# Performance work log

Hardware: AMD Instinct MI355X
Metric: run time of the kernel (lower is better)

Reference implementation:

```python
import jax, jax.numpy as jnp
import numpy as np

EPS = 1e-12  # torch F.normalize eps

def _l2norm(v, axis):
    n = jnp.linalg.norm(v, axis=axis, keepdims=True)
    return v / jnp.maximum(n, EPS)

def setup_inputs() -> dict:
    key = jax.random.key(0)
    k1, k2, k3 = jax.random.split(key, 3)
    N, D, H, W, K = 32, 512, 40, 40, 64
    x = jax.random.normal(k1, (N, D, H, W), dtype=jnp.float32)
    conv_weight = jax.random.normal(k2, (K, D), dtype=jnp.float32) * 0.05
    centroids = jax.random.uniform(k3, (K, D), dtype=jnp.float32)
    return {"x": x, "conv_weight": conv_weight, "centroids": centroids}

def reference(x, conv_weight, centroids):
    N, D, H, W = x.shape
    K = centroids.shape[0]
    # descriptor-wise L2 normalization over channel dim
    x = _l2norm(x, axis=1)
    x_flat = x.reshape(N, D, H * W)                       # [N, D, S]
    # 1x1 conv == per-pixel linear: [K,D] @ [N,D,S] -> [N,K,S]
    logits = jnp.einsum('kd,nds->nks', conv_weight, x_flat)
    soft_assign = jax.nn.softmax(logits, axis=1)          # softmax over clusters
    # vlad[n,k,d] = sum_s a[n,k,s] * (x[n,d,s] - c[k,d])
    #            = (a @ x^T) - (sum_s a) * c   -- two GEMM-like ops, no K-loop
    agg = jnp.einsum('nks,nds->nkd', soft_assign, x_flat)  # [N, K, D]
    a_sum = soft_assign.sum(axis=2)                        # [N, K]
    vlad = agg - a_sum[:, :, None] * centroids[None, :, :]
    # intra-normalization over D, flatten, global L2 normalization
    vlad = _l2norm(vlad, axis=2)
    vlad = vlad.reshape(N, K * D)
    vlad = _l2norm(vlad, axis=1)
    return vlad
```

## Files before the change

kernel.cpp:

```cpp
#include <hip/hip_runtime.h>
#include <math.h>

#define N_ 32
#define D_ 512
#define S_ 1600
#define K_ 64

typedef __attribute__((ext_vector_type(8))) short short8;
typedef __attribute__((ext_vector_type(4))) short short4v;
typedef __attribute__((ext_vector_type(4))) float f32x4;
typedef __attribute__((ext_vector_type(2))) unsigned u32x2;

static __device__ __forceinline__ short f2bf(float f) {
    unsigned u = __float_as_uint(f);
    u += 0x7fffu + ((u >> 16) & 1u);
    return (short)(u >> 16);
}
static __device__ __forceinline__ unsigned pk2(float a, float b) {
    return (unsigned)(unsigned short)f2bf(a) | ((unsigned)(unsigned short)f2bf(b) << 16);
}

__global__ __launch_bounds__(256) void kW(const float* __restrict__ w,
                                          short* __restrict__ w16)
{
    int i4 = (blockIdx.x * 256 + threadIdx.x) * 4;
    float4 v = *(const float4*)&w[i4];
    short4 h = {f2bf(v.x), f2bf(v.y), f2bf(v.z), f2bf(v.w)};
    *(short4*)&w16[i4] = h;
}

__global__ __launch_bounds__(256) void kA(const float* __restrict__ x,
                                          const short* __restrict__ w16,
                                          short* __restrict__ aprime,
                                          float* __restrict__ asum)
{
    __shared__ short T[2][64 * 64];
    __shared__ float invSS[64];
    __shared__ float wredS[4][66];

    const int tid = threadIdx.x;
    const int wv  = tid >> 6;
    const int l   = tid & 63;
    const int lk  = l & 15;
    const int q   = l >> 4;
    const int n   = blockIdx.x / 25;
    const int s0  = (blockIdx.x % 25) * 64;

    const float* xb = x + (size_t)n * D_ * S_;
    const float* xrow = xb + (size_t)(4 * wv + q) * S_ + s0 + 4 * lk;
    const int row   = 4 * lk + q;
    const int rswz  = row & 15;

    float ssql[4] = {0.f, 0.f, 0.f, 0.f};
    f32x4 accl[4];
#pragma unroll
    for (int st = 0; st < 4; ++st) accl[st] = (f32x4){0.f, 0.f, 0.f, 0.f};

    if (tid < 64) invSS[tid] = 0.f;

#define STAGE(c, b)                                                          \
    {                                                                        \
        float4 v[4];                                                         \
        _Pragma("unroll")                                                    \
        for (int jj = 0; jj < 4; ++jj)                                       \
            v[jj] = *(const float4*)&xrow[(size_t)(64 * (c) + 16 * jj) * S_];\
        _Pragma("unroll")                                                    \
        for (int jj = 0; jj < 4; ++jj) {                                     \
            ssql[0] += v[jj].x * v[jj].x;  ssql[1] += v[jj].y * v[jj].y;     \
            ssql[2] += v[jj].z * v[jj].z;  ssql[3] += v[jj].w * v[jj].w;     \
            unsigned p0 = pk2(v[jj].x, v[jj].y), p1 = pk2(v[jj].z, v[jj].w); \
            unsigned mine = (l & 32) ? p0 : p1;                              \
            unsigned oth  = (unsigned)__shfl_xor((int)mine, 32);             \
            unsigned a0 = (l & 32) ? oth : p0;                               \
            unsigned a1 = (l & 32) ? p1 : oth;                               \
            unsigned r0 = (unsigned)__shfl_xor((int)a0, 16);                 \
            unsigned r1 = (unsigned)__shfl_xor((int)a1, 16);                 \
            unsigned o0, o1;                                                 \
            if (l & 16) {                                                    \
                o0 = (r0 >> 16) | (a0 & 0xffff0000u);                        \
                o1 = (r1 >> 16) | (a1 & 0xffff0000u);                        \
            } else {                                                         \
                o0 = (a0 & 0xffffu) | (r0 << 16);                            \
                o1 = (a1 & 0xffffu) | (r1 << 16);                            \
            }                                                                \
            *(u32x2*)&T[b][row * 64 + (((4 * jj + wv) ^ rswz) << 2)] =       \
                (u32x2){o0, o1};                                             \
        }                                                                    \
    }

    STAGE(0, 0);
    __syncthreads();

    for (int c = 0; c < 8; ++c) {
        if (c < 7) {
            if ((c & 1) == 0) STAGE(c + 1, 1) else STAGE(c + 1, 0)
        }
        const int b = c & 1;
#pragma unroll
        for (int kl = 0; kl < 2; ++kl) {
            short8 af = *(const short8*)&w16[(size_t)(16 * wv + lk) * D_
                                             + 64 * c + 32 * kl + 8 * q];
#pragma unroll
            for (int st = 0; st < 4; ++st) {
                const int rr = st * 16 + lk;
                const int c4 = 8 * kl + 2 * q;
                short4v pa = *(const short4v*)&T[b][rr * 64 + (((c4    ) ^ (rr & 15)) << 2)];
                short4v pb = *(const short4v*)&T[b][rr * 64 + (((c4 + 1) ^ (rr & 15)) << 2)];
                short8 bf = {pa[0], pa[1], pa[2], pa[3], pb[0], pb[1], pb[2], pb[3]};
                accl[st] = __builtin_amdgcn_mfma_f32_16x16x32_bf16(af, bf, accl[st], 0, 0, 0);
            }
        }
        if (c == 7) {
#pragma unroll
            for (int i = 0; i < 4; ++i) {
                ssql[i] += __shfl_xor(ssql[i], 16);
                ssql[i] += __shfl_xor(ssql[i], 32);
            }
            if (q == 0) {
#pragma unroll
                for (int i = 0; i < 4; ++i) atomicAdd(&invSS[4 * lk + i], ssql[i]);
            }
        }
        __syncthreads();
    }
#undef STAGE

    float e[4][4], invv[4];
#pragma unroll
    for (int st = 0; st < 4; ++st) {
        invv[st] = 1.0f / fmaxf(sqrtf(invSS[st * 16 + lk]), 1e-12f);
        float sm = 0.f;
#pragma unroll
        for (int r = 0; r < 4; ++r) {
            e[st][r] = __expf(accl[st][r] * invv[st]);
            sm += e[st][r];
        }
        sm += __shfl_xor(sm, 16);
        sm += __shfl_xor(sm, 32);
        if (q == 0) wredS[wv][st * 16 + lk] = sm;
    }
    __syncthreads();

    float asum_loc[4] = {0.f, 0.f, 0.f, 0.f};
    short* apb = aprime + (size_t)n * K_ * S_ + s0;
#pragma unroll
    for (int st = 0; st < 4; ++st) {
        const int s = st * 16 + lk;
        const float rs = 1.0f / (wredS[0][s] + wredS[1][s]
                               + wredS[2][s] + wredS[3][s]);
#pragma unroll
        for (int r = 0; r < 4; ++r) {
            const float p = e[st][r] * rs;
            apb[(size_t)(16 * wv + 4 * q + r) * S_ + s] = f2bf(p * invv[st]);
            asum_loc[r] += p;
        }
    }
#pragma unroll
    for (int r = 0; r < 4; ++r) {
        float v = asum_loc[r];
        v += __shfl_xor(v, 1);  v += __shfl_xor(v, 2);
        v += __shfl_xor(v, 4);  v += __shfl_xor(v, 8);
        if (lk == 0) atomicAdd(&asum[n * K_ + 16 * wv + 4 * q + r], v);
    }
}

__global__ __launch_bounds__(256) void kB(const float* __restrict__ x,
                                          const short* __restrict__ aprime,
                                          float* __restrict__ agg)
{
    const int bid = blockIdx.x;
    const int n  = bid / 40;
    const int dt = (bid % 40) / 10;
    const int sp = bid % 10;
    const int wv = threadIdx.x >> 6;
    const int l  = threadIdx.x & 63;
    const int lk = l & 15;
    const int q  = l >> 4;
    const int dbase = dt * 128 + wv * 32;

    const short* ap = aprime + (size_t)n * K_ * S_;
    const float* xb = x + (size_t)n * D_ * S_;

    f32x4 acc[4][2];
#pragma unroll
    for (int kt = 0; kt < 4; ++kt)
#pragma unroll
        for (int ds = 0; ds < 2; ++ds) acc[kt][ds] = (f32x4){0.f, 0.f, 0.f, 0.f};

#pragma unroll
    for (int kst = 0; kst < 5; ++kst) {
        const int s = sp * 160 + kst * 32 + q * 8;
        short8 af[4];
#pragma unroll
        for (int kt = 0; kt < 4; ++kt)
            af[kt] = *(const short8*)&ap[(size_t)(kt * 16 + lk) * S_ + s];
        short8 bf[2];
#pragma unroll
        for (int ds = 0; ds < 2; ++ds) {
            const float* xp = &xb[(size_t)(dbase + ds * 16 + lk) * S_ + s];
            float4 v0 = *(const float4*)xp;
            float4 v1 = *(const float4*)(xp + 4);
            short8 b;
            b[0] = f2bf(v0.x); b[1] = f2bf(v0.y); b[2] = f2bf(v0.z); b[3] = f2bf(v0.w);
            b[4] = f2bf(v1.x); b[5] = f2bf(v1.y); b[6] = f2bf(v1.z); b[7] = f2bf(v1.w);
            bf[ds] = b;
        }
#pragma unroll
        for (int kt = 0; kt < 4; ++kt)
#pragma unroll
            for (int ds = 0; ds < 2; ++ds)
                acc[kt][ds] = __builtin_amdgcn_mfma_f32_16x16x32_bf16(af[kt], bf[ds], acc[kt][ds], 0, 0, 0);
    }

    float* ab = agg + (size_t)n * K_ * D_;
#pragma unroll
    for (int kt = 0; kt < 4; ++kt)
#pragma unroll
        for (int ds = 0; ds < 2; ++ds)
#pragma unroll
            for (int r = 0; r < 4; ++r)
                atomicAdd(&ab[(size_t)(kt * 16 + 4 * q + r) * D_ + dbase + ds * 16 + lk],
                          acc[kt][ds][r]);
}

__global__ __launch_bounds__(256) void kC(const float* __restrict__ agg,
                                          const float* __restrict__ asum,
                                          const float* __restrict__ cent,
                                          float* __restrict__ out)
{
    __shared__ float red[4];
    const int tid = threadIdx.x;
    const int nk = blockIdx.x;
    const int k = nk & 63;
    const float as = asum[nk];
    const float* cb = cent + (size_t)k * D_;
    const float* ag = agg + (size_t)nk * D_;

    float v0 = ag[tid]       - as * cb[tid];
    float v1 = ag[tid + 256] - as * cb[tid + 256];
    float ssq = v0 * v0 + v1 * v1;

    ssq += __shfl_xor(ssq, 32);
    ssq += __shfl_xor(ssq, 16);
    ssq += __shfl_xor(ssq, 8);
    ssq += __shfl_xor(ssq, 4);
    ssq += __shfl_xor(ssq, 2);
    ssq += __shfl_xor(ssq, 1);
    if ((tid & 63) == 0) red[tid >> 6] = ssq;
    __syncthreads();
    const float total = red[0] + red[1] + red[2] + red[3];
    const float scale = 1.0f / (fmaxf(sqrtf(total), 1e-12f) * 8.0f);

    out[(size_t)nk * D_ + tid]       = v0 * scale;
    out[(size_t)nk * D_ + tid + 256] = v1 * scale;
}

extern "C" void kernel_launch(void* const* d_in, const int* in_sizes, int n_in,
                              void* d_out, int out_size, void* d_ws, size_t ws_size,
                              hipStream_t stream)
{
    const float* x    = (const float*)d_in[0];
    const float* w    = (const float*)d_in[1];
    const float* cent = (const float*)d_in[2];
    float* out = (float*)d_out;

    float* agg    = (float*)d_ws;
    float* asum   = agg + (size_t)N_ * K_ * D_;
    short* aprime = (short*)(asum + N_ * K_);
    short* w16    = aprime + (size_t)N_ * K_ * S_;

    hipMemsetAsync(agg, 0, ((size_t)N_ * K_ * D_ + N_ * K_) * sizeof(float), stream);

    kW<<<32, 256, 0, stream>>>(w, w16);
    kA<<<N_ * (S_ / 64), 256, 0, stream>>>(x, w16, aprime, asum);
    kB<<<N_ * 4 * 10, 256, 0, stream>>>(x, aprime, agg);
    kC<<<N_ * K_, 256, 0, stream>>>(agg, asum, cent, out);
}
```

Measured before the change: 219.9 us.

## Halve kA spatial tile to 32 pixels and split load/store for pipelining

The logits/softmax kernel now processes 32 spatial positions per block instead of 64, doubling the grid to 1600 blocks so more CUs are busy. Staging is split into a global-load step issued before the MFMA loop and a transpose/LDS-store step after it, so load latency overlaps compute. It also moves the sum-of-squares reduction out of the loop and drops the final per-iteration barrier. Each block does less work, so the W fragment reloads and per-block overhead grow relative to the useful work.

Result: no change. 218.8 us (-0.5%).

```diff
diff --git a/kernel.cpp b/kernel.cpp
--- a/kernel.cpp
+++ b/kernel.cpp
@@ -34,100 +34,111 @@
                                           short* __restrict__ aprime,
                                           float* __restrict__ asum)
 {
-    __shared__ short T[2][64 * 64];
-    __shared__ float invSS[64];
-    __shared__ float wredS[4][66];
+    __shared__ short T[2][32 * 64];
+    __shared__ float invSS[32];
+    __shared__ float wredS[4][34];
 
     const int tid = threadIdx.x;
     const int wv  = tid >> 6;
     const int l   = tid & 63;
     const int lk  = l & 15;
     const int q   = l >> 4;
-    const int n   = blockIdx.x / 25;
-    const int s0  = (blockIdx.x % 25) * 64;
+    const int n   = blockIdx.x / 50;
+    const int s0  = (blockIdx.x % 50) * 32;
 
     const float* xb = x + (size_t)n * D_ * S_;
-    const float* xrow = xb + (size_t)(4 * wv + q) * S_ + s0 + 4 * lk;
-    const int row   = 4 * lk + q;
-    const int rswz  = row & 15;
+    const float* xrow = xb + (size_t)(4 * (lk >> 3) + q) * S_ + s0 + 4 * (lk & 7);
+    const int row  = 4 * (lk & 7) + q;
+    const int rsw  = row & 15;
 
     float ssql[4] = {0.f, 0.f, 0.f, 0.f};
-    f32x4 accl[4];
-#pragma unroll
-    for (int st = 0; st < 4; ++st) accl[st] = (f32x4){0.f, 0.f, 0.f, 0.f};
-
-    if (tid < 64) invSS[tid] = 0.f;
-
-#define STAGE(c, b)                                                          \
+    f32x4 accl[2];
+    accl[0] = (f32x4){0.f, 0.f, 0.f, 0.f};
+    accl[1] = accl[0];
+
+    if (tid < 32) invSS[tid] = 0.f;
+
+    float4 v0, v1;
+#define LOADC(c)                                                             \
     {                                                                        \
-        float4 v[4];                                                         \
-        _Pragma("unroll")                                                    \
-        for (int jj = 0; jj < 4; ++jj)                                       \
-            v[jj] = *(const float4*)&xrow[(size_t)(64 * (c) + 16 * jj) * S_];\
-        _Pragma("unroll")                                                    \
-        for (int jj = 0; jj < 4; ++jj) {                                     \
-            ssql[0] += v[jj].x * v[jj].x;  ssql[1] += v[jj].y * v[jj].y;     \
-            ssql[2] += v[jj].z * v[jj].z;  ssql[3] += v[jj].w * v[jj].w;     \
-            unsigned p0 = pk2(v[jj].x, v[jj].y), p1 = pk2(v[jj].z, v[jj].w); \
-            unsigned mine = (l & 32) ? p0 : p1;                              \
-            unsigned oth  = (unsigned)__shfl_xor((int)mine, 32);             \
-            unsigned a0 = (l & 32) ? oth : p0;                               \
-            unsigned a1 = (l & 32) ? p1 : oth;                               \
-            unsigned r0 = (unsigned)__shfl_xor((int)a0, 16);                 \
-            unsigned r1 = (unsigned)__shfl_xor((int)a1, 16);                 \
-            unsigned o0, o1;                                                 \
-            if (l & 16) {                                                    \
-                o0 = (r0 >> 16) | (a0 & 0xffff0000u);                        \
-                o1 = (r1 >> 16) | (a1 & 0xffff0000u);                        \
-            } else {                                                         \
-                o0 = (a0 & 0xffffu) | (r0 << 16);                            \
-                o1 = (a1 & 0xffffu) | (r1 << 16);                            \
-            }                                                                \
-            *(u32x2*)&T[b][row * 64 + (((4 * jj + wv) ^ rswz) << 2)] =       \
-                (u32x2){o0, o1};                                             \
+        v0 = *(const float4*)&xrow[(size_t)(64 * (c) + 8 * wv) * S_];        \
+        v1 = *(const float4*)&xrow[(size_t)(64 * (c) + 8 * wv + 32) * S_];   \
+    }
+#define TRN(v, b, c4)                                                        \
+    {                                                                        \
+        ssql[0] += v.x * v.x;  ssql[1] += v.y * v.y;                         \
+        ssql[2] += v.z * v.z;  ssql[3] += v.w * v.w;                         \
+        unsigned p0 = pk2(v.x, v.y), p1 = pk2(v.z, v.w);                     \
+        unsigned mine = (l & 32) ? p0 : p1;                                  \
+        unsigned oth  = (unsigned)__shfl_xor((int)mine, 32);                 \
+        unsigned a0 = (l & 32) ? oth : p0;                                   \
+        unsigned a1 = (l & 32) ? p1 : oth;                                   \
+        unsigned r0 = (unsigned)__shfl_xor((int)a0, 16);                     \
+        unsigned r1 = (unsigned)__shfl_xor((int)a1, 16);                     \
+        unsigned o0, o1;                                                     \
+        if (l & 16) {                                                        \
+            o0 = (r0 >> 16) | (a0 & 0xffff0000u);                            \
+            o1 = (r1 >> 16) | (a1 & 0xffff0000u);                            \
+        } else {                                                             \
+            o0 = (a0 & 0xffffu) | (r0 << 16);                                \
+            o1 = (a1 & 0xffffu) | (r1 << 16);                                \
         }                                                                    \
-    }
-
-    STAGE(0, 0);
-    __syncthreads();
-
+        *(u32x2*)&T[b][row * 64 + ((((c4)) ^ rsw) << 2)] = (u32x2){o0, o1};  \
+    }
+#define STOREC(b)                                                            \
+    {                                                                        \
+        TRN(v0, b, 2 * wv + (lk >> 3));                                      \
+        TRN(v1, b, 2 * (wv + 4) + (lk >> 3));                                \
+    }
+
+    LOADC(0);
+    STOREC(0);
+    __syncthreads();
+
+#pragma unroll
     for (int c = 0; c < 8; ++c) {
-        if (c < 7) {
-            if ((c & 1) == 0) STAGE(c + 1, 1) else STAGE(c + 1, 0)
-        }
+        if (c < 7) LOADC(c + 1);
+
         const int b = c & 1;
+        const short* wbase = w16 + (size_t)(16 * wv + lk) * D_ + 64 * c + 8 * q;
 #pragma unroll
         for (int kl = 0; kl < 2; ++kl) {
-            short8 af = *(const short8*)&w16[(size_t)(16 * wv + lk) * D_
-                                             + 64 * c + 32 * kl + 8 * q];
-#pragma unroll
-            for (int st = 0; st < 4; ++st) {
+            short8 af = *(const short8*)&wbase[32 * kl];
+#pragma unroll
+            for (int st = 0; st < 2; ++st) {
                 const int rr = st * 16 + lk;
                 const int c4 = 8 * kl + 2 * q;
-                short4v pa = *(const short4v*)&T[b][rr * 64 + (((c4    ) ^ (rr & 15)) << 2)];
-                short4v pb = *(const short4v*)&T[b][rr * 64 + (((c4 + 1) ^ (rr & 15)) << 2)];
+                short4v pa = *(const short4v*)&T[b][rr * 64 + (((c4    ) ^ lk) << 2)];
+                short4v pb = *(const short4v*)&T[b][rr * 64 + (((c4 + 1) ^ lk) << 2)];
                 short8 bf = {pa[0], pa[1], pa[2], pa[3], pb[0], pb[1], pb[2], pb[3]};
                 accl[st] = __builtin_amdgcn_mfma_f32_16x16x32_bf16(af, bf, accl[st], 0, 0, 0);
             }
         }
-        if (c == 7) {
-#pragma unroll
-            for (int i = 0; i < 4; ++i) {
-                ssql[i] += __shfl_xor(ssql[i], 16);
-                ssql[i] += __shfl_xor(ssql[i], 32);
-            }
-            if (q == 0) {
-#pragma unroll
-                for (int i = 0; i < 4; ++i) atomicAdd(&invSS[4 * lk + i], ssql[i]);
-            }
-        }
-        __syncthreads();
-    }
-#undef STAGE
-
-    float e[4][4], invv[4];
-#pragma unroll
-    for (int st = 0; st < 4; ++st) {
+
+        if (c < 7) {
+            STOREC((c + 1) & 1);
+            __syncthreads();
+        }
+    }
+#undef LOADC
+#undef TRN
+#undef STOREC
+
+#pragma unroll
+    for (int i = 0; i < 4; ++i) {
+        ssql[i] += __shfl_xor(ssql[i], 16);
+        ssql[i] += __shfl_xor(ssql[i], 32);
+        ssql[i] += __shfl_xor(ssql[i], 8);
+    }
+    if (l < 8) {
+#pragma unroll
+        for (int i = 0; i < 4; ++i) atomicAdd(&invSS[4 * l + i], ssql[i]);
+    }
+    __syncthreads();
+
+    float e[2][4], invv[2];
+#pragma unroll
+    for (int st = 0; st < 2; ++st) {
         invv[st] = 1.0f / fmaxf(sqrtf(invSS[st * 16 + lk]), 1e-12f);
         float sm = 0.f;
 #pragma unroll
@@ -144,7 +155,7 @@
     float asum_loc[4] = {0.f, 0.f, 0.f, 0.f};
     short* apb = aprime + (size_t)n * K_ * S_ + s0;
 #pragma unroll
-    for (int st = 0; st < 4; ++st) {
+    for (int st = 0; st < 2; ++st) {
         const int s = st * 16 + lk;
         const float rs = 1.0f / (wredS[0][s] + wredS[1][s]
                                + wredS[2][s] + wredS[3][s]);
@@ -272,7 +283,7 @@
     hipMemsetAsync(agg, 0, ((size_t)N_ * K_ * D_ + N_ * K_) * sizeof(float), stream);
 
     kW<<<32, 256, 0, stream>>>(w, w16);
-    kA<<<N_ * (S_ / 64), 256, 0, stream>>>(x, w16, aprime, asum);
+    kA<<<N_ * (S_ / 32), 256, 0, stream>>>(x, w16, aprime, asum);
     kB<<<N_ * 4 * 10, 256, 0, stream>>>(x, aprime, agg);
     kC<<<N_ * K_, 256, 0, stream>>>(agg, asum, cent, out);
 }
```
